# Performance work log

Hardware: AMD Instinct MI355X
Metric: run time of the kernel (lower is better)

The kernel has to match this reference:

```python
import jax, jax.numpy as jnp
import numpy as np
from jax import lax

B, NH, NW, C, H = 8, 32, 32, 384, 12
N = NH * NW
HD = C // H
HID = 2 * C
SCALE = HD ** -0.5
EPS = 1e-5


def _rel_index(nh, nw):
    coords = np.stack(np.meshgrid(np.arange(nh), np.arange(nw), indexing='ij'))  # [2,nh,nw]
    cf = coords.reshape(2, -1)                      # [2, N]
    rel = (cf[:, :, None] - cf[:, None, :]).transpose(1, 2, 0).astype(np.int64)  # [N,N,2]
    rel[:, :, 0] += nh - 1
    rel[:, :, 1] += nw - 1
    rel[:, :, 0] *= 2 * nw - 1
    return jnp.asarray(rel.sum(-1), dtype=jnp.int32)  # [N,N]


def setup_inputs() -> dict:
    key = jax.random.key(0)
    ks = jax.random.split(key, 10)
    nrel = (2 * NH - 1) * (2 * NW - 1)
    return {
        'x': jax.random.normal(ks[0], (B, N, C), jnp.float32),
        'n_h': NH,
        'n_w': NW,
        'rel_index': _rel_index(NH, NW),
        'ln1_g': jnp.ones((C,), jnp.float32),
        'ln1_b': jnp.zeros((C,), jnp.float32),
        'w_qkv': jax.random.normal(ks[1], (3 * C, C), jnp.float32) * 0.02,
        'w_proj': jax.random.normal(ks[2], (C, C), jnp.float32) * 0.02,
        'b_proj': jnp.zeros((C,), jnp.float32),
        'rel_table': jax.random.normal(ks[3], (nrel, H), jnp.float32) * 0.02,
        'global_bias': jax.random.normal(ks[4], (max(N, 1024), max(N, 1024)), jnp.float32) * 0.02,
        'ln2_g': jnp.ones((C,), jnp.float32),
        'ln2_b': jnp.zeros((C,), jnp.float32),
        'w_pw1': jax.random.normal(ks[5], (HID, C, 1, 1), jnp.float32) * 0.05,
        'b_pw1': jnp.zeros((HID,), jnp.float32),
        'w_dw': jax.random.normal(ks[6], (HID, 1, 3, 3), jnp.float32) * 0.05,
        'b_dw': jnp.zeros((HID,), jnp.float32),
        'w_pw2': jax.random.normal(ks[7], (C, HID, 1, 1), jnp.float32) * 0.05,
        'b_pw2': jnp.zeros((C,), jnp.float32),
    }


def _layernorm(x, g, b):
    m = jnp.mean(x, axis=-1, keepdims=True)
    v = jnp.mean((x - m) ** 2, axis=-1, keepdims=True)
    return (x - m) * lax.rsqrt(v + EPS) * g + b


def _conv(x, w, b, pad, dil, groups):
    y = lax.conv_general_dilated(x, w, window_strides=(1, 1),
                                 padding=[(pad, pad), (pad, pad)],
                                 rhs_dilation=(dil, dil),
                                 dimension_numbers=('NCHW', 'OIHW', 'NCHW'),
                                 feature_group_count=groups)
    return y + b[None, :, None, None]


def _mlp(x, n_h, n_w, w_pw1, b_pw1, w_dw, b_dw, w_pw2, b_pw2):
    b, n, c = x.shape
    fmap = x.transpose(0, 2, 1).reshape(b, c, n_h, n_w)          # tokens -> map
    y = _conv(fmap, w_pw1, b_pw1, 0, 1, 1)                       # 1x1
    y = jax.nn.gelu(y, approximate=False)
    y = _conv(y, w_dw, b_dw, 2, 2, HID)                          # depthwise dilated 3x3
    y = jax.nn.gelu(y, approximate=False)
    y = _conv(y, w_pw2, b_pw2, 0, 1, 1)                          # 1x1
    return y.reshape(b, c, n).transpose(0, 2, 1)                 # map -> tokens


def _attn(x, rel_index, w_qkv, w_proj, b_proj, rel_table, global_bias):
    b, n, c = x.shape
    qkv = (x @ w_qkv.T).reshape(b, n, 3, H, HD).transpose(2, 0, 3, 1, 4)  # [3,B,H,N,HD]
    q, k, v = qkv[0], qkv[1], qkv[2]
    scores = jnp.einsum('bhqd,bhkd->bhqk', q, k) * SCALE
    rpb = rel_table[rel_index].transpose(2, 0, 1)                # [H,N,N]
    gb = global_bias[:n, :n]                                     # [N,N]
    scores = scores + rpb[None] + gb[None, None]
    attn = jax.nn.softmax(scores, axis=-1)
    out = jnp.einsum('bhqk,bhkd->bhqd', attn, v).transpose(0, 2, 1, 3).reshape(b, n, c)
    return out @ w_proj.T + b_proj


def reference(x, n_h, n_w, rel_index, ln1_g, ln1_b, w_qkv, w_proj, b_proj,
              rel_table, global_bias, ln2_g, ln2_b,
              w_pw1, b_pw1, w_dw, b_dw, w_pw2, b_pw2):
    # forward order in source: MLP block first, then attention block
    x = x + _mlp(_layernorm(x, ln2_g, ln2_b), n_h, n_w, w_pw1, b_pw1, w_dw, b_dw, w_pw2, b_pw2)
    x = x + _attn(_layernorm(x, ln1_g, ln1_b), rel_index, w_qkv, w_proj, b_proj, rel_table, global_bias)
    return x
```

## Files before the change

kernel.cpp:

```cpp
#include <hip/hip_runtime.h>
#include <cstdint>
#include <cstddef>

using ushort_t = unsigned short;

#define DEVI __device__ __forceinline__

typedef __attribute__((ext_vector_type(8))) __bf16 bf16x8;
typedef __attribute__((ext_vector_type(4))) float f32x4;
typedef __attribute__((ext_vector_type(8))) unsigned short u16x8;
typedef __attribute__((ext_vector_type(4))) unsigned short u16x4;

DEVI ushort_t f2bf(float f) {
  unsigned u = __builtin_bit_cast(unsigned, f);
  u += 0x7FFFu + ((u >> 16) & 1u);
  return (ushort_t)(u >> 16);
}
DEVI float bf2f(ushort_t h) {
  unsigned u = ((unsigned)h) << 16;
  return __builtin_bit_cast(float, u);
}
DEVI bf16x8 ldb8(const ushort_t* p) {
  return __builtin_bit_cast(bf16x8, *(const u16x8*)p);
}
DEVI float geluf(float x) { return 0.5f * x * (1.0f + erff(x * 0.70710678118654752f)); }

DEVI void gload16(const void* g, void* l) {
  __builtin_amdgcn_global_load_lds((const __attribute__((address_space(1))) void*)g,
                                   (__attribute__((address_space(3))) void*)l, 16, 0, 0);
}

#define SCALE_Q 0.17677669529663689f

__global__ __launch_bounds__(256) void convert_k(
    const float* __restrict__ wqkv, const float* __restrict__ wproj,
    const float* __restrict__ wpw1, const float* __restrict__ wpw2,
    const float* __restrict__ wdw,
    ushort_t* __restrict__ o_qkv, ushort_t* __restrict__ o_proj,
    ushort_t* __restrict__ o_pw1, ushort_t* __restrict__ o_pw2,
    ushort_t* __restrict__ o_dwt) {
  int i = blockIdx.x * 256 + threadIdx.x;
  if (i < 442368) { o_qkv[i] = f2bf(wqkv[i]); return; }
  i -= 442368;
  if (i < 147456) { o_proj[i] = f2bf(wproj[i]); return; }
  i -= 147456;
  if (i < 294912) { o_pw1[i] = f2bf(wpw1[i]); return; }
  i -= 294912;
  if (i < 294912) { o_pw2[i] = f2bf(wpw2[i]); return; }
  i -= 294912;
  const int c = i / 9, tap = i % 9;
  o_dwt[tap * 768 + c] = f2bf(wdw[i]);
}

__global__ __launch_bounds__(256) void ln_k(const float* __restrict__ x,
                                            const float* __restrict__ g,
                                            const float* __restrict__ bta,
                                            ushort_t* __restrict__ out) {
  const int w = threadIdx.x >> 6, l = threadIdx.x & 63;
  const size_t row = (size_t)blockIdx.x * 4 + w;
  const float* xr = x + row * 384;
  float v[6];
  float s = 0.f;
#pragma unroll
  for (int i = 0; i < 6; i++) { v[i] = xr[i * 64 + l]; s += v[i]; }
#pragma unroll
  for (int off = 32; off; off >>= 1) s += __shfl_xor(s, off);
  const float mean = s * (1.0f / 384.0f);
  float q2 = 0.f;
#pragma unroll
  for (int i = 0; i < 6; i++) { const float d = v[i] - mean; q2 += d * d; }
#pragma unroll
  for (int off = 32; off; off >>= 1) q2 += __shfl_xor(q2, off);
  const float rstd = rsqrtf(q2 * (1.0f / 384.0f) + 1e-5f);
  ushort_t* orow = out + row * 384;
#pragma unroll
  for (int i = 0; i < 6; i++) {
    const int c = i * 64 + l;
    orow[c] = f2bf((v[i] - mean) * rstd * g[c] + bta[c]);
  }
}

__global__ __launch_bounds__(256) void dwconv_k(const ushort_t* __restrict__ y1,
                                                const ushort_t* __restrict__ wdwt,
                                                const float* __restrict__ bdw,
                                                ushort_t* __restrict__ y2) {
  const int tid = blockIdx.x * 256 + threadIdx.x;
  const int cg = tid % 96;
  const int pix = (tid / 96) & 1023;
  const int b_ = tid / (96 * 1024);
  const int hh = pix >> 5, ww = pix & 31;
  const int c0 = cg * 8;
  float acc[8];
#pragma unroll
  for (int j = 0; j < 8; j++) acc[j] = bdw[c0 + j];
#pragma unroll
  for (int kh = 0; kh < 3; kh++) {
    const int h2 = hh + 2 * kh - 2;
    if ((unsigned)h2 >= 32u) continue;
#pragma unroll
    for (int kw = 0; kw < 3; kw++) {
      const int w2 = ww + 2 * kw - 2;
      if ((unsigned)w2 >= 32u) continue;
      const u16x8 iv = *(const u16x8*)&y1[((size_t)(b_ << 10) + (h2 << 5) + w2) * 768 + c0];
      const u16x8 wv = *(const u16x8*)&wdwt[(kh * 3 + kw) * 768 + c0];
#pragma unroll
      for (int j = 0; j < 8; j++) acc[j] += bf2f(iv[j]) * bf2f(wv[j]);
    }
  }
  u16x8 ov;
#pragma unroll
  for (int j = 0; j < 8; j++) ov[j] = f2bf(geluf(acc[j]));
  *(u16x8*)&y2[((size_t)(b_ << 10) + pix) * 768 + c0] = ov;
}

__global__ __launch_bounds__(256) void biaspre_k(const int* __restrict__ ridx,
                                                 const float* __restrict__ rtab,
                                                 const float* __restrict__ gb,
                                                 ushort_t* __restrict__ biasf) {
  const int lin = blockIdx.x * 256 + threadIdx.x;
  const int l = lin & 63, k16 = (lin >> 6) & 63, q16 = lin >> 12;
  const int lg = l >> 4, lr = l & 15;
  const int q = q16 * 16 + lr, k0 = k16 * 16 + lg * 4;
  const int4 iv = *(const int4*)&ridx[q * 1024 + k0];
  const float4 gv = *(const float4*)&gb[q * 1024 + k0];
  const int idx[4] = {iv.x, iv.y, iv.z, iv.w};
  const float g4[4] = {gv.x, gv.y, gv.z, gv.w};
  float rv[4][12];
#pragma unroll
  for (int r = 0; r < 4; r++) {
    const float4 t0 = *(const float4*)&rtab[idx[r] * 12];
    const float4 t1 = *(const float4*)&rtab[idx[r] * 12 + 4];
    const float4 t2 = *(const float4*)&rtab[idx[r] * 12 + 8];
    rv[r][0] = t0.x; rv[r][1] = t0.y; rv[r][2] = t0.z; rv[r][3] = t0.w;
    rv[r][4] = t1.x; rv[r][5] = t1.y; rv[r][6] = t1.z; rv[r][7] = t1.w;
    rv[r][8] = t2.x; rv[r][9] = t2.y; rv[r][10] = t2.z; rv[r][11] = t2.w;
  }
#pragma unroll
  for (int h = 0; h < 12; h++) {
    u16x4 ov;
#pragma unroll
    for (int r = 0; r < 4; r++) ov[r] = f2bf(rv[r][h] + g4[r]);
    *(u16x4*)&biasf[(((size_t)(h * 64 + q16) * 64 + k16) * 64 + l) * 4] = ov;
  }
}

template <int BM, int BN, int MR, int NR, int EPI>
__global__ __launch_bounds__(256) void gemm_k(
    const ushort_t* __restrict__ A, const ushort_t* __restrict__ Bw, int K, int Ncols,
    const float* __restrict__ bias, const float* __restrict__ resid,
    void* __restrict__ o0, void* __restrict__ o1, void* __restrict__ o2) {
  constexpr int WN = BN / (16 * NR);
  constexpr int WM = BM / (16 * MR);
  static_assert(WM * WN == 4, "4 waves");
  constexpr int ABUF = BM * 32, BBUF = BN * 32, BUFSZ = ABUF + BBUF;
  __shared__ ushort_t smem[2 * BUFSZ];
  const int tid = threadIdx.x, w = tid >> 6, l = tid & 63;
  const int lg = l >> 4, lr = l & 15;
  constexpr int MT = 8192 / BM;
  const int mt = blockIdx.x % MT, nt = blockIdx.x / MT;
  const int trow = mt * BM, tcol = nt * BN;
  const int wr = w / WN, wc = w % WN;

  f32x4 acc[MR][NR];
#pragma unroll
  for (int m = 0; m < MR; m++)
#pragma unroll
    for (int n = 0; n < NR; n++) acc[m][n] = (f32x4){0.f, 0.f, 0.f, 0.f};

  auto stage = [&](int buf, int k0) {
    ushort_t* sb = &smem[buf * BUFSZ];
#pragma unroll
    for (int u0 = 0; u0 < BM * 4; u0 += 256) {
      const int u = u0 + tid;
      const int row = u >> 2, slot = (u & 3) ^ ((row >> 1) & 3);
      gload16(A + (size_t)(trow + row) * K + k0 + slot * 8, sb + (u0 + w * 64) * 8);
    }
    ushort_t* sbB = sb + ABUF;
#pragma unroll
    for (int u0 = 0; u0 < BN * 4; u0 += 256) {
      const int u = u0 + tid;
      const int row = u >> 2, slot = (u & 3) ^ ((row >> 1) & 3);
      gload16(Bw + (size_t)(tcol + row) * K + k0 + slot * 8, sbB + (u0 + w * 64) * 8);
    }
  };

  const int nsteps = K >> 5;
  stage(0, 0);
  __syncthreads();
  for (int t = 0; t < nsteps; t++) {
    if (t + 1 < nsteps) stage((t + 1) & 1, (t + 1) << 5);
    const int bo = (t & 1) * BUFSZ;
    bf16x8 af[MR], bfr[NR];
#pragma unroll
    for (int m = 0; m < MR; m++) {
      const int ra = wr * (MR * 16) + m * 16 + lr;
      af[m] = ldb8(&smem[bo + ra * 32 + ((lg ^ ((ra >> 1) & 3)) << 3)]);
    }
#pragma unroll
    for (int n = 0; n < NR; n++) {
      const int rb = wc * (NR * 16) + n * 16 + lr;
      bfr[n] = ldb8(&smem[bo + ABUF + rb * 32 + ((lg ^ ((rb >> 1) & 3)) << 3)]);
    }
#pragma unroll
    for (int m = 0; m < MR; m++)
#pragma unroll
      for (int n = 0; n < NR; n++)
        acc[m][n] = __builtin_amdgcn_mfma_f32_16x16x32_bf16(af[m], bfr[n], acc[m][n], 0, 0, 0);
    __syncthreads();
  }

#pragma unroll
  for (int m = 0; m < MR; m++) {
    const int rowb = trow + wr * (MR * 16) + m * 16 + lg * 4;
#pragma unroll
    for (int n = 0; n < NR; n++) {
      const int col = tcol + wc * (NR * 16) + n * 16 + lr;
#pragma unroll
      for (int r = 0; r < 4; r++) {
        const float v = acc[m][n][r];
        const int rw = rowb + r;
        if constexpr (EPI == 0) {
          ((ushort_t*)o0)[(size_t)rw * Ncols + col] = f2bf(geluf(v + bias[col]));
        } else if constexpr (EPI == 1) {
          ((float*)o0)[(size_t)rw * 384 + col] =
              resid[(size_t)rw * 384 + col] + v + bias[col];
        } else {
          const int sel = col / 384, c2 = col % 384, hh = c2 >> 5, d = c2 & 31;
          const int b_ = rw >> 10, nn = rw & 1023;
          const size_t bh = (size_t)(b_ * 12 + hh);
          if (sel == 0) {
            ((ushort_t*)o0)[(bh * 1024 + nn) * 32 + d] = f2bf(v * SCALE_Q);
          } else if (sel == 1) {
            ((ushort_t*)o1)[(bh * 1024 + nn) * 32 + (d & 7) +
                            (((d >> 3) ^ ((nn >> 1) & 3)) << 3)] = f2bf(v);
          } else {
            const int kt = nn >> 6, rem = nn & 63, p = rem >> 5, ks = rem & 31;
            const int lgv = (ks & 15) >> 2, jv = ((ks >> 4) << 2) | (ks & 3);
            const int dh = d >> 4, lrv = d & 15;
            ((ushort_t*)o2)[bh * 32768 + kt * 2048 + (p * 2 + dh) * 512 +
                            (lgv * 16 + lrv) * 8 + jv] = f2bf(v);
          }
        }
      }
    }
  }
}

__global__ __launch_bounds__(256) void attn_k(const ushort_t* __restrict__ Q,
                                              const ushort_t* __restrict__ Kb,
                                              const ushort_t* __restrict__ Vt,
                                              const ushort_t* __restrict__ biasf,
                                              ushort_t* __restrict__ AO) {
  __shared__ ushort_t smem[16384];
  const int tid = threadIdx.x, w = tid >> 6, l = tid & 63, lg = l >> 4, lr = l & 15;
  const int L = (blockIdx.x & 7) * 192 + (blockIdx.x >> 3);
  const int h = L >> 7, rem = L & 127, b_ = rem >> 4, qb = rem & 15;
  const int q16 = qb * 4 + w, qrow0 = q16 << 4;
  const size_t bh = (size_t)(b_ * 12 + h);
  const ushort_t* kb = Kb + bh * 32768;
  const ushort_t* vbf = Vt + bh * 32768;
  const ushort_t* bbq = biasf + (size_t)(h * 64 + q16) * 16384;
  const bf16x8 qf = ldb8(Q + (bh * 1024 + qrow0 + lr) * 32 + lg * 8);

  auto stage = [&](int buf, int kt) {
    ushort_t* base = &smem[buf * 8192];
    gload16(kb + (kt << 6) * 32 + w * 512 + l * 8, base + w * 512);
    gload16(vbf + kt * 2048 + w * 512 + l * 8, base + 2048 + w * 512);
    gload16(bbq + kt * 1024 + l * 8, base + 4096 + w * 1024);
    gload16(bbq + kt * 1024 + 512 + l * 8, base + 4096 + w * 1024 + 512);
  };

  f32x4 o0 = {0.f, 0.f, 0.f, 0.f}, o1 = {0.f, 0.f, 0.f, 0.f};
  float mrun = -1e30f, lsum = 0.f;

  stage(0, 0);
  asm volatile("s_waitcnt vmcnt(0)");
  __syncthreads();

  for (int kt = 0; kt < 16; kt++) {
    const int buf = kt & 1;
    if (kt < 15) stage(buf ^ 1, kt + 1);
    const ushort_t* base = &smem[buf * 8192];
    f32x4 s[4];
#pragma unroll
    for (int kf = 0; kf < 4; kf++) {
      const bf16x8 kfr =
          ldb8(base + (kf * 16 + lr) * 32 + ((lg ^ ((lr >> 1) & 3)) << 3));
      const u16x4 b4 = *(const u16x4*)(base + 4096 + w * 1024 + kf * 256 + l * 4);
      f32x4 c;
#pragma unroll
      for (int r = 0; r < 4; r++) c[r] = bf2f(b4[r]);
      s[kf] = __builtin_amdgcn_mfma_f32_16x16x32_bf16(kfr, qf, c, 0, 0, 0);
    }
    float tm = s[0][0];
#pragma unroll
    for (int kf = 0; kf < 4; kf++)
#pragma unroll
      for (int r = 0; r < 4; r++) tm = fmaxf(tm, s[kf][r]);
    tm = fmaxf(tm, __shfl_xor(tm, 16));
    tm = fmaxf(tm, __shfl_xor(tm, 32));
    if (!__all(tm - mrun <= 8.f)) {
      const float nm = fmaxf(mrun, tm);
      const float sc = __expf(mrun - nm);
      mrun = nm;
      lsum *= sc;
      float scr[4];
#pragma unroll
      for (int r = 0; r < 4; r++) scr[r] = __shfl(sc, lg * 4 + r);
#pragma unroll
      for (int r = 0; r < 4; r++) { o0[r] *= scr[r]; o1[r] *= scr[r]; }
    }
    float rs = 0.f;
#pragma unroll
    for (int kf = 0; kf < 4; kf++)
#pragma unroll
      for (int r = 0; r < 4; r++) { s[kf][r] = __expf(s[kf][r] - mrun); rs += s[kf][r]; }
    rs += __shfl_xor(rs, 16);
    rs += __shfl_xor(rs, 32);
    lsum += rs;
#pragma unroll
    for (int p = 0; p < 2; p++) {
      bf16x8 pa;
#pragma unroll
      for (int j = 0; j < 4; j++) {
        pa[j] = (__bf16)s[2 * p][j];
        pa[4 + j] = (__bf16)s[2 * p + 1][j];
      }
      o0 = __builtin_amdgcn_mfma_f32_16x16x32_bf16(
          pa, ldb8(base + 2048 + (p * 2 + 0) * 512 + l * 8), o0, 0, 0, 0);
      o1 = __builtin_amdgcn_mfma_f32_16x16x32_bf16(
          pa, ldb8(base + 2048 + (p * 2 + 1) * 512 + l * 8), o1, 0, 0, 0);
    }
    if (kt < 15) {
      asm volatile("s_waitcnt vmcnt(0)");
      __syncthreads();
    }
  }
  float linv[4];
#pragma unroll
  for (int r = 0; r < 4; r++) linv[r] = 1.0f / __shfl(lsum, lg * 4 + r);
#pragma unroll
  for (int r = 0; r < 4; r++) {
    const size_t rowb = ((size_t)(b_ << 10) + qrow0 + lg * 4 + r) * 384 + h * 32;
    AO[rowb + lr] = f2bf(o0[r] * linv[r]);
    AO[rowb + 16 + lr] = f2bf(o1[r] * linv[r]);
  }
}

constexpr size_t WS_WQKV = 0;
constexpr size_t WS_WPROJ = WS_WQKV + 884736;
constexpr size_t WS_WPW1 = WS_WPROJ + 294912;
constexpr size_t WS_WPW2 = WS_WPW1 + 589824;
constexpr size_t WS_WDWT = WS_WPW2 + 589824;
constexpr size_t WS_XLN = WS_WDWT + 16384;
constexpr size_t WS_Y1 = WS_XLN + 6291456;
constexpr size_t WS_Y2 = WS_Y1 + 12582912;
constexpr size_t WS_X1 = WS_Y2 + 12582912;
constexpr size_t WS_Q = WS_X1 + 12582912;
constexpr size_t WS_K = WS_Q + 6291456;
constexpr size_t WS_VT = WS_K + 6291456;
constexpr size_t WS_BIAS = WS_VT + 6291456;
constexpr size_t WS_AO = WS_BIAS + 25165824;

extern "C" void kernel_launch(void* const* d_in, const int* in_sizes, int n_in,
                              void* d_out, int out_size, void* d_ws, size_t ws_size,
                              hipStream_t stream) {
  (void)in_sizes; (void)n_in; (void)out_size; (void)ws_size;
  const float* x = (const float*)d_in[0];
  const int* rel_index = (const int*)d_in[3];
  const float* ln1_g = (const float*)d_in[4];
  const float* ln1_b = (const float*)d_in[5];
  const float* w_qkv = (const float*)d_in[6];
  const float* w_proj = (const float*)d_in[7];
  const float* b_proj = (const float*)d_in[8];
  const float* rel_table = (const float*)d_in[9];
  const float* gbias = (const float*)d_in[10];
  const float* ln2_g = (const float*)d_in[11];
  const float* ln2_b = (const float*)d_in[12];
  const float* w_pw1 = (const float*)d_in[13];
  const float* b_pw1 = (const float*)d_in[14];
  const float* w_dw = (const float*)d_in[15];
  const float* b_dw = (const float*)d_in[16];
  const float* w_pw2 = (const float*)d_in[17];
  const float* b_pw2 = (const float*)d_in[18];
  float* out = (float*)d_out;

  char* ws = (char*)d_ws;
  ushort_t* wq_bf = (ushort_t*)(ws + WS_WQKV);
  ushort_t* wp_bf = (ushort_t*)(ws + WS_WPROJ);
  ushort_t* w1_bf = (ushort_t*)(ws + WS_WPW1);
  ushort_t* w2_bf = (ushort_t*)(ws + WS_WPW2);
  ushort_t* wdwt = (ushort_t*)(ws + WS_WDWT);
  ushort_t* xln = (ushort_t*)(ws + WS_XLN);
  ushort_t* y1 = (ushort_t*)(ws + WS_Y1);
  ushort_t* y2 = (ushort_t*)(ws + WS_Y2);
  float* x1f = (float*)(ws + WS_X1);
  ushort_t* qb = (ushort_t*)(ws + WS_Q);
  ushort_t* kbuf = (ushort_t*)(ws + WS_K);
  ushort_t* vtb = (ushort_t*)(ws + WS_VT);
  ushort_t* biasf = (ushort_t*)(ws + WS_BIAS);
  ushort_t* ao = (ushort_t*)(ws + WS_AO);

  convert_k<<<4635, 256, 0, stream>>>(w_qkv, w_proj, w_pw1, w_pw2, w_dw,
                                      wq_bf, wp_bf, w1_bf, w2_bf, wdwt);
  biaspre_k<<<1024, 256, 0, stream>>>(rel_index, rel_table, gbias, biasf);

  ln_k<<<2048, 256, 0, stream>>>(x, ln2_g, ln2_b, xln);
  gemm_k<64, 64, 2, 2, 0><<<1536, 256, 0, stream>>>(xln, w1_bf, 384, 768, b_pw1,
                                                    nullptr, y1, nullptr, nullptr);
  dwconv_k<<<3072, 256, 0, stream>>>(y1, wdwt, b_dw, y2);
  gemm_k<64, 64, 2, 2, 1><<<768, 256, 0, stream>>>(y2, w2_bf, 768, 384, b_pw2, x,
                                                   x1f, nullptr, nullptr);

  ln_k<<<2048, 256, 0, stream>>>(x1f, ln1_g, ln1_b, xln);
  gemm_k<64, 64, 2, 2, 2><<<2304, 256, 0, stream>>>(xln, wq_bf, 384, 1152, nullptr,
                                                    nullptr, qb, kbuf, vtb);
  attn_k<<<1536, 256, 0, stream>>>(qb, kbuf, vtb, biasf, ao);
  gemm_k<64, 64, 2, 2, 1><<<768, 256, 0, stream>>>(ao, wp_bf, 384, 384, b_proj, x1f,
                                                   out, nullptr, nullptr);
}
```

Before: 232.8 us.

## Process two query tiles per wave in attention and switch softmax to exp2

Each attention wave now handles two 16-row query tiles that share the same staged K/V fragments. This halves the grid and the K/V LDS traffic per query row, and it hoists the K and V fragment loads out of the inner loops. Softmax now uses exp2, with log2(e) folded into the Q scale and the precomputed bias, and the row max uses v_max3. The cost is higher register and LDS use per block and fewer blocks to hide latency. The threshold-8 rescale check is now in log2 units, which changes its effective tolerance.

```diff
diff --git a/kernel.cpp b/kernel.cpp
--- a/kernel.cpp
+++ b/kernel.cpp
@@ -29,8 +29,15 @@
   __builtin_amdgcn_global_load_lds((const __attribute__((address_space(1))) void*)g,
                                    (__attribute__((address_space(3))) void*)l, 16, 0, 0);
 }
-
-#define SCALE_Q 0.17677669529663689f
+DEVI float fmax3(float a, float b, float c) {
+  float r;
+  asm("v_max3_f32 %0, %1, %2, %3" : "=v"(r) : "v"(a), "v"(b), "v"(c));
+  return r;
+}
+DEVI float exp2a(float x) { return exp2f(x); }
+
+#define LOG2E 1.4426950408889634f
+#define SCALE_QL 0.2550348281f
 
 __global__ __launch_bounds__(256) void convert_k(
     const float* __restrict__ wqkv, const float* __restrict__ wproj,
@@ -139,7 +146,7 @@
   for (int h = 0; h < 12; h++) {
     u16x4 ov;
 #pragma unroll
-    for (int r = 0; r < 4; r++) ov[r] = f2bf(rv[r][h] + g4[r]);
+    for (int r = 0; r < 4; r++) ov[r] = f2bf((rv[r][h] + g4[r]) * LOG2E);
     *(u16x4*)&biasf[(((size_t)(h * 64 + q16) * 64 + k16) * 64 + l) * 4] = ov;
   }
 }
@@ -229,7 +236,7 @@
           const int b_ = rw >> 10, nn = rw & 1023;
           const size_t bh = (size_t)(b_ * 12 + hh);
           if (sel == 0) {
-            ((ushort_t*)o0)[(bh * 1024 + nn) * 32 + d] = f2bf(v * SCALE_Q);
+            ((ushort_t*)o0)[(bh * 1024 + nn) * 32 + d] = f2bf(v * SCALE_QL);
           } else if (sel == 1) {
             ((ushort_t*)o1)[(bh * 1024 + nn) * 32 + (d & 7) +
                             (((d >> 3) ^ ((nn >> 1) & 3)) << 3)] = f2bf(v);
@@ -251,27 +258,32 @@
                                               const ushort_t* __restrict__ Vt,
                                               const ushort_t* __restrict__ biasf,
                                               ushort_t* __restrict__ AO) {
-  __shared__ ushort_t smem[16384];
+  __shared__ ushort_t smem[24576];
   const int tid = threadIdx.x, w = tid >> 6, l = tid & 63, lg = l >> 4, lr = l & 15;
-  const int L = (blockIdx.x & 7) * 192 + (blockIdx.x >> 3);
-  const int h = L >> 7, rem = L & 127, b_ = rem >> 4, qb = rem & 15;
-  const int q16 = qb * 4 + w, qrow0 = q16 << 4;
+  const int L = (blockIdx.x & 7) * 96 + (blockIdx.x >> 3);
+  const int h = L >> 6, rem = L & 63, b_ = rem >> 3, qb = rem & 7;
+  const int q16A = qb * 8 + w, q16B = q16A + 4;
+  const int qrow0A = q16A << 4, qrow0B = q16B << 4;
   const size_t bh = (size_t)(b_ * 12 + h);
   const ushort_t* kb = Kb + bh * 32768;
   const ushort_t* vbf = Vt + bh * 32768;
-  const ushort_t* bbq = biasf + (size_t)(h * 64 + q16) * 16384;
-  const bf16x8 qf = ldb8(Q + (bh * 1024 + qrow0 + lr) * 32 + lg * 8);
+  const ushort_t* bbA = biasf + (size_t)(h * 64 + q16A) * 16384;
+  const ushort_t* bbB = biasf + (size_t)(h * 64 + q16B) * 16384;
+  const bf16x8 qfA = ldb8(Q + (bh * 1024 + qrow0A + lr) * 32 + lg * 8);
+  const bf16x8 qfB = ldb8(Q + (bh * 1024 + qrow0B + lr) * 32 + lg * 8);
 
   auto stage = [&](int buf, int kt) {
-    ushort_t* base = &smem[buf * 8192];
+    ushort_t* base = &smem[buf * 12288];
     gload16(kb + (kt << 6) * 32 + w * 512 + l * 8, base + w * 512);
     gload16(vbf + kt * 2048 + w * 512 + l * 8, base + 2048 + w * 512);
-    gload16(bbq + kt * 1024 + l * 8, base + 4096 + w * 1024);
-    gload16(bbq + kt * 1024 + 512 + l * 8, base + 4096 + w * 1024 + 512);
+    gload16(bbA + kt * 1024 + l * 8, base + 4096 + w * 2048);
+    gload16(bbA + kt * 1024 + 512 + l * 8, base + 4096 + w * 2048 + 512);
+    gload16(bbB + kt * 1024 + l * 8, base + 4096 + w * 2048 + 1024);
+    gload16(bbB + kt * 1024 + 512 + l * 8, base + 4096 + w * 2048 + 1536);
   };
 
-  f32x4 o0 = {0.f, 0.f, 0.f, 0.f}, o1 = {0.f, 0.f, 0.f, 0.f};
-  float mrun = -1e30f, lsum = 0.f;
+  f32x4 oA0 = {0.f, 0.f, 0.f, 0.f}, oA1 = oA0, oB0 = oA0, oB1 = oA0;
+  float mA = -1e30f, lA = 0.f, mB = -1e30f, lB = 0.f;
 
   stage(0, 0);
   asm volatile("s_waitcnt vmcnt(0)");
@@ -280,70 +292,105 @@
   for (int kt = 0; kt < 16; kt++) {
     const int buf = kt & 1;
     if (kt < 15) stage(buf ^ 1, kt + 1);
-    const ushort_t* base = &smem[buf * 8192];
-    f32x4 s[4];
+    const ushort_t* base = &smem[buf * 12288];
+    bf16x8 kfr[4];
+#pragma unroll
+    for (int kf = 0; kf < 4; kf++)
+      kfr[kf] = ldb8(base + (kf * 16 + lr) * 32 + ((lg ^ ((lr >> 1) & 3)) << 3));
+    bf16x8 vfr[4];
+#pragma unroll
+    for (int dv = 0; dv < 4; dv++) vfr[dv] = ldb8(base + 2048 + dv * 512 + l * 8);
+    f32x4 sA[4], sB[4];
 #pragma unroll
     for (int kf = 0; kf < 4; kf++) {
-      const bf16x8 kfr =
-          ldb8(base + (kf * 16 + lr) * 32 + ((lg ^ ((lr >> 1) & 3)) << 3));
-      const u16x4 b4 = *(const u16x4*)(base + 4096 + w * 1024 + kf * 256 + l * 4);
-      f32x4 c;
-#pragma unroll
-      for (int r = 0; r < 4; r++) c[r] = bf2f(b4[r]);
-      s[kf] = __builtin_amdgcn_mfma_f32_16x16x32_bf16(kfr, qf, c, 0, 0, 0);
-    }
-    float tm = s[0][0];
+      const u16x4 b4A = *(const u16x4*)(base + 4096 + w * 2048 + kf * 256 + l * 4);
+      const u16x4 b4B = *(const u16x4*)(base + 4096 + w * 2048 + 1024 + kf * 256 + l * 4);
+      f32x4 cA, cB;
+#pragma unroll
+      for (int r = 0; r < 4; r++) { cA[r] = bf2f(b4A[r]); cB[r] = bf2f(b4B[r]); }
+      sA[kf] = __builtin_amdgcn_mfma_f32_16x16x32_bf16(kfr[kf], qfA, cA, 0, 0, 0);
+      sB[kf] = __builtin_amdgcn_mfma_f32_16x16x32_bf16(kfr[kf], qfB, cB, 0, 0, 0);
+    }
+    float tA, tB;
+    {
+      const float u0 = fmax3(sA[0][0], sA[0][1], sA[0][2]);
+      const float u1 = fmax3(sA[0][3], sA[1][0], sA[1][1]);
+      const float u2 = fmax3(sA[1][2], sA[1][3], sA[2][0]);
+      const float u3 = fmax3(sA[2][1], sA[2][2], sA[2][3]);
+      const float u4 = fmax3(sA[3][0], sA[3][1], sA[3][2]);
+      tA = fmaxf(fmax3(u0, u1, u2), fmax3(u3, u4, sA[3][3]));
+      const float v0 = fmax3(sB[0][0], sB[0][1], sB[0][2]);
+      const float v1 = fmax3(sB[0][3], sB[1][0], sB[1][1]);
+      const float v2 = fmax3(sB[1][2], sB[1][3], sB[2][0]);
+      const float v3 = fmax3(sB[2][1], sB[2][2], sB[2][3]);
+      const float v4 = fmax3(sB[3][0], sB[3][1], sB[3][2]);
+      tB = fmaxf(fmax3(v0, v1, v2), fmax3(v3, v4, sB[3][3]));
+    }
+    tA = fmaxf(tA, __shfl_xor(tA, 16));
+    tA = fmaxf(tA, __shfl_xor(tA, 32));
+    tB = fmaxf(tB, __shfl_xor(tB, 16));
+    tB = fmaxf(tB, __shfl_xor(tB, 32));
+    if (!__all((tA - mA <= 8.f) && (tB - mB <= 8.f))) {
+      const float nmA = fmaxf(mA, tA), nmB = fmaxf(mB, tB);
+      const float scA = exp2a(mA - nmA), scB = exp2a(mB - nmB);
+      mA = nmA; mB = nmB; lA *= scA; lB *= scB;
+#pragma unroll
+      for (int r = 0; r < 4; r++) {
+        const float sa = __shfl(scA, lg * 4 + r), sb = __shfl(scB, lg * 4 + r);
+        oA0[r] *= sa; oA1[r] *= sa; oB0[r] *= sb; oB1[r] *= sb;
+      }
+    }
 #pragma unroll
     for (int kf = 0; kf < 4; kf++)
 #pragma unroll
-      for (int r = 0; r < 4; r++) tm = fmaxf(tm, s[kf][r]);
-    tm = fmaxf(tm, __shfl_xor(tm, 16));
-    tm = fmaxf(tm, __shfl_xor(tm, 32));
-    if (!__all(tm - mrun <= 8.f)) {
-      const float nm = fmaxf(mrun, tm);
-      const float sc = __expf(mrun - nm);
-      mrun = nm;
-      lsum *= sc;
-      float scr[4];
-#pragma unroll
-      for (int r = 0; r < 4; r++) scr[r] = __shfl(sc, lg * 4 + r);
-#pragma unroll
-      for (int r = 0; r < 4; r++) { o0[r] *= scr[r]; o1[r] *= scr[r]; }
-    }
-    float rs = 0.f;
-#pragma unroll
-    for (int kf = 0; kf < 4; kf++)
-#pragma unroll
-      for (int r = 0; r < 4; r++) { s[kf][r] = __expf(s[kf][r] - mrun); rs += s[kf][r]; }
-    rs += __shfl_xor(rs, 16);
-    rs += __shfl_xor(rs, 32);
-    lsum += rs;
+      for (int r = 0; r < 4; r++) {
+        sA[kf][r] = exp2a(sA[kf][r] - mA);
+        sB[kf][r] = exp2a(sB[kf][r] - mB);
+      }
+    float rsA = ((sA[0][0] + sA[0][1]) + (sA[0][2] + sA[0][3])) +
+                ((sA[1][0] + sA[1][1]) + (sA[1][2] + sA[1][3])) +
+                (((sA[2][0] + sA[2][1]) + (sA[2][2] + sA[2][3])) +
+                 ((sA[3][0] + sA[3][1]) + (sA[3][2] + sA[3][3])));
+    float rsB = ((sB[0][0] + sB[0][1]) + (sB[0][2] + sB[0][3])) +
+                ((sB[1][0] + sB[1][1]) + (sB[1][2] + sB[1][3])) +
+                (((sB[2][0] + sB[2][1]) + (sB[2][2] + sB[2][3])) +
+                 ((sB[3][0] + sB[3][1]) + (sB[3][2] + sB[3][3])));
+    rsA += __shfl_xor(rsA, 16);
+    rsA += __shfl_xor(rsA, 32);
+    rsB += __shfl_xor(rsB, 16);
+    rsB += __shfl_xor(rsB, 32);
+    lA += rsA;
+    lB += rsB;
 #pragma unroll
     for (int p = 0; p < 2; p++) {
-      bf16x8 pa;
+      bf16x8 paA, paB;
 #pragma unroll
       for (int j = 0; j < 4; j++) {
-        pa[j] = (__bf16)s[2 * p][j];
-        pa[4 + j] = (__bf16)s[2 * p + 1][j];
+        paA[j] = (__bf16)sA[2 * p][j];
+        paA[4 + j] = (__bf16)sA[2 * p + 1][j];
+        paB[j] = (__bf16)sB[2 * p][j];
+        paB[4 + j] = (__bf16)sB[2 * p + 1][j];
       }
-      o0 = __builtin_amdgcn_mfma_f32_16x16x32_bf16(
-          pa, ldb8(base + 2048 + (p * 2 + 0) * 512 + l * 8), o0, 0, 0, 0);
-      o1 = __builtin_amdgcn_mfma_f32_16x16x32_bf16(
-          pa, ldb8(base + 2048 + (p * 2 + 1) * 512 + l * 8), o1, 0, 0, 0);
+      oA0 = __builtin_amdgcn_mfma_f32_16x16x32_bf16(paA, vfr[p * 2 + 0], oA0, 0, 0, 0);
+      oA1 = __builtin_amdgcn_mfma_f32_16x16x32_bf16(paA, vfr[p * 2 + 1], oA1, 0, 0, 0);
+      oB0 = __builtin_amdgcn_mfma_f32_16x16x32_bf16(paB, vfr[p * 2 + 0], oB0, 0, 0, 0);
+      oB1 = __builtin_amdgcn_mfma_f32_16x16x32_bf16(paB, vfr[p * 2 + 1], oB1, 0, 0, 0);
     }
     if (kt < 15) {
       asm volatile("s_waitcnt vmcnt(0)");
       __syncthreads();
     }
   }
-  float linv[4];
-#pragma unroll
-  for (int r = 0; r < 4; r++) linv[r] = 1.0f / __shfl(lsum, lg * 4 + r);
 #pragma unroll
   for (int r = 0; r < 4; r++) {
-    const size_t rowb = ((size_t)(b_ << 10) + qrow0 + lg * 4 + r) * 384 + h * 32;
-    AO[rowb + lr] = f2bf(o0[r] * linv[r]);
-    AO[rowb + 16 + lr] = f2bf(o1[r] * linv[r]);
+    const float liA = 1.0f / __shfl(lA, lg * 4 + r);
+    const float liB = 1.0f / __shfl(lB, lg * 4 + r);
+    const size_t rowA = ((size_t)(b_ << 10) + qrow0A + lg * 4 + r) * 384 + h * 32;
+    const size_t rowB = ((size_t)(b_ << 10) + qrow0B + lg * 4 + r) * 384 + h * 32;
+    AO[rowA + lr] = f2bf(oA0[r] * liA);
+    AO[rowA + 16 + lr] = f2bf(oA1[r] * liA);
+    AO[rowB + lr] = f2bf(oB0[r] * liB);
+    AO[rowB + 16 + lr] = f2bf(oB1[r] * liB);
   }
 }
 
@@ -415,7 +462,7 @@
   ln_k<<<2048, 256, 0, stream>>>(x1f, ln1_g, ln1_b, xln);
   gemm_k<64, 64, 2, 2, 2><<<2304, 256, 0, stream>>>(xln, wq_bf, 384, 1152, nullptr,
                                                     nullptr, qb, kbuf, vtb);
-  attn_k<<<1536, 256, 0, stream>>>(qb, kbuf, vtb, biasf, ao);
+  attn_k<<<768, 256, 0, stream>>>(qb, kbuf, vtb, biasf, ao);
   gemm_k<64, 64, 2, 2, 1><<<768, 256, 0, stream>>>(ao, wp_bf, 384, 384, b_proj, x1f,
                                                    out, nullptr, nullptr);
 }
```

Result: slower. 239.7 us (+3.0%).
